# Kernel optimization log

Measured on AMD Instinct MI355X. Metric: run time of the kernel, lower is better.

Reference implementation:

```python
import jax, jax.numpy as jnp
import numpy as np

DIST_THRESH = 0.5   # stands in for config.dist_thresh
ALPHA = 0.2         # LeakyReLU negative slope
NEG_INF = -9e15     # mask value used by the original module


def setup_inputs() -> dict:
    key = jax.random.key(0)
    k1, k2, k3 = jax.random.split(key, 3)
    N, dim = 8192, 128
    nodes = jax.random.normal(k1, (N, dim), dtype=jnp.float32)
    dist = jax.random.uniform(k2, (N, N), dtype=jnp.float32)
    # xavier_uniform on (2*dim, 1) with gain 1.414
    limit = 1.414 * np.sqrt(6.0 / (2 * dim + 1))
    a = jax.random.uniform(k3, (2 * dim, 1), dtype=jnp.float32,
                           minval=-limit, maxval=limit)
    return {"nodes": nodes, "dist": dist, "a": a}


def reference(nodes, dist, a):
    # Original math: e_ij = leakyrelu([h_i || h_j] @ a). Since a = [a1; a2],
    # this equals leakyrelu(h_i @ a1 + h_j @ a2) — same values, no N^2*2dim tensor.
    dim = nodes.shape[1]
    a1 = a[:dim, 0]                      # [dim]
    a2 = a[dim:, 0]                      # [dim]
    s1 = nodes @ a1                      # [N] — contribution of row node i
    s2 = nodes @ a2                      # [N] — contribution of col node j
    e = jax.nn.leaky_relu(s1[:, None] + s2[None, :], negative_slope=ALPHA)  # [N, N]
    masked = jnp.where(dist < DIST_THRESH, e, NEG_INF)
    attention = jax.nn.softmax(masked, axis=1)   # [N, N]
    h_prime = attention @ nodes                  # [N, dim]
    return h_prime
```

## Files before the change

kernel.cpp:

```cpp
#include <hip/hip_runtime.h>
#include <stdint.h>

#define NN 8192
#define DIM 128
#define ALPHA 0.2f
#define MTILE 32
#define BTHREADS 512

typedef float f32x16 __attribute__((ext_vector_type(16)));
typedef short bf16x8 __attribute__((ext_vector_type(8)));

__device__ __forceinline__ float b2f(uint32_t u){
  uint32_t x = u << 16;
  float f;
  __builtin_memcpy(&f, &x, 4);
  return f;
}
__device__ __forceinline__ uint16_t f2b(float f){
  uint32_t x;
  __builtin_memcpy(&x, &f, 4);
  x += 0x7FFFu + ((x >> 16) & 1u);
  return (uint16_t)(x >> 16);
}

__global__ void s_kernel(const float* __restrict__ nodes,
                         const float* __restrict__ a,
                         float* __restrict__ s1, float* __restrict__ s2){
  int row  = blockIdx.x * 4 + (threadIdx.x >> 6);
  int lane = threadIdx.x & 63;
  float2 nv  = *(const float2*)(nodes + row * DIM + lane * 2);
  float2 a1v = *(const float2*)(a + lane * 2);
  float2 a2v = *(const float2*)(a + DIM + lane * 2);
  float p1 = nv.x * a1v.x + nv.y * a1v.y;
  float p2 = nv.x * a2v.x + nv.y * a2v.y;
  #pragma unroll
  for (int off = 32; off; off >>= 1){
    p1 += __shfl_down(p1, off);
    p2 += __shfl_down(p2, off);
  }
  if (lane == 0){ s1[row] = p1; s2[row] = p2; }
}

__global__ void t_kernel(const float* __restrict__ nodes,
                         uint16_t* __restrict__ nodesT){
  __shared__ uint16_t tile[32][33];
  int kb = blockIdx.x * 32, nb = blockIdx.y * 32;
  int tx = threadIdx.x & 31, ty = threadIdx.x >> 5;
  for (int r = ty; r < 32; r += 8)
    tile[r][tx] = f2b(nodes[(size_t)(kb + r) * DIM + nb + tx]);
  __syncthreads();
  for (int r = ty; r < 32; r += 8)
    nodesT[(size_t)(nb + r) * NN + kb + tx] = tile[tx][r];
}

__global__ void __launch_bounds__(BTHREADS)
attn_kernel(const float* __restrict__ dist,
            const uint16_t* __restrict__ nodesT,
            const float* __restrict__ s1,
            const float* __restrict__ s2,
            float* __restrict__ out){
  const int tid  = threadIdx.x;
  const int wave = tid >> 6;
  const int lane = tid & 63;
  const int m    = lane & 31;
  const int half = lane >> 5;
  const int i0   = blockIdx.x * MTILE;

  const float s1v = s1[i0 + m];

  const int kwave = NN / (BTHREADS / 64);
  const int kbeg  = wave * kwave;
  const int steps = kwave / 16;

  f32x16 acc0, acc1, acc2, acc3;
  #pragma unroll
  for (int i = 0; i < 16; i++){ acc0[i] = 0.f; acc1[i] = 0.f; acc2[i] = 0.f; acc3[i] = 0.f; }
  float den = 0.f;

  const float*    dp  = dist   + (size_t)(i0 + m) * NN + kbeg + half * 8;
  const float*    sp  = s2     + kbeg + half * 8;
  const uint16_t* b0p = nodesT + (size_t)m * NN + kbeg + half * 8;
  const uint16_t* b1p = b0p + (size_t)32 * NN;
  const uint16_t* b2p = b0p + (size_t)64 * NN;
  const uint16_t* b3p = b0p + (size_t)96 * NN;

  for (int s = 0; s < steps; s++){
    float4 da  = *(const float4*)dp;
    float4 db  = *(const float4*)(dp + 4);
    float4 sa  = *(const float4*)sp;
    float4 sb  = *(const float4*)(sp + 4);
    uint4  nb0 = *(const uint4*)b0p;
    uint4  nb1 = *(const uint4*)b1p;
    uint4  nb2 = *(const uint4*)b2p;
    uint4  nb3 = *(const uint4*)b3p;

    float dv[8]  = {da.x, da.y, da.z, da.w, db.x, db.y, db.z, db.w};
    float s2v[8] = {sa.x, sa.y, sa.z, sa.w, sb.x, sb.y, sb.z, sb.w};

    union { bf16x8 v; uint16_t u[8]; } af;
    #pragma unroll
    for (int j = 0; j < 8; j++){
      float x = s1v + s2v[j];
      float e = fmaxf(x, ALPHA * x);
      float w = (dv[j] < 0.5f) ? __expf(e) : 0.f;
      uint16_t wq = f2b(w);
      af.u[j] = wq;
      den += b2f((uint32_t)wq);
    }

    acc0 = __builtin_amdgcn_mfma_f32_32x32x16_bf16(af.v, *(const bf16x8*)&nb0, acc0, 0, 0, 0);
    acc1 = __builtin_amdgcn_mfma_f32_32x32x16_bf16(af.v, *(const bf16x8*)&nb1, acc1, 0, 0, 0);
    acc2 = __builtin_amdgcn_mfma_f32_32x32x16_bf16(af.v, *(const bf16x8*)&nb2, acc2, 0, 0, 0);
    acc3 = __builtin_amdgcn_mfma_f32_32x32x16_bf16(af.v, *(const bf16x8*)&nb3, acc3, 0, 0, 0);

    dp  += 16; sp  += 16;
    b0p += 16; b1p += 16; b2p += 16; b3p += 16;
  }

  __shared__ float accT[MTILE][DIM];
  __shared__ float denT[MTILE];
  for (int idx = tid; idx < MTILE * DIM; idx += BTHREADS) ((float*)accT)[idx] = 0.f;
  if (tid < MTILE) denT[tid] = 0.f;
  __syncthreads();

  #pragma unroll
  for (int r = 0; r < 16; r++){
    int row = (r & 3) + 8 * (r >> 2) + 4 * half;
    atomicAdd(&accT[row][ 0 + m], acc0[r]);
    atomicAdd(&accT[row][32 + m], acc1[r]);
    atomicAdd(&accT[row][64 + m], acc2[r]);
    atomicAdd(&accT[row][96 + m], acc3[r]);
  }
  atomicAdd(&denT[m], den);
  __syncthreads();

  if (tid < MTILE) denT[tid] = 1.0f / denT[tid];
  __syncthreads();

  for (int idx = tid; idx < MTILE * DIM; idx += BTHREADS){
    int row = idx >> 7, col = idx & 127;
    out[(size_t)(i0 + row) * DIM + col] = accT[row][col] * denT[row];
  }
}

extern "C" void kernel_launch(void* const* d_in, const int* in_sizes, int n_in,
                              void* d_out, int out_size, void* d_ws, size_t ws_size,
                              hipStream_t stream){
  const float* nodes = (const float*)d_in[0];
  const float* dist  = (const float*)d_in[1];
  const float* a     = (const float*)d_in[2];
  float* out = (float*)d_out;

  char* ws = (char*)d_ws;
  float*    s1     = (float*)ws;
  float*    s2     = (float*)(ws + (32 << 10));
  uint16_t* nodesT = (uint16_t*)(ws + (64 << 10));

  s_kernel<<<NN / 4, 256, 0, stream>>>(nodes, a, s1, s2);
  t_kernel<<<dim3(NN / 32, DIM / 32), 256, 0, stream>>>(nodes, nodesT);
  attn_kernel<<<NN / MTILE, BTHREADS, 0, stream>>>(dist, nodesT, s1, s2, out);
}
```

Measured before the change: 471.6 us.

## Split the K dimension of the attention kernel across blocks with global atomic reduction

Adds a second grid dimension that splits the 8192-long key range into four chunks, so the attention kernel launches four times as many blocks. Each block reduces its partial numerator and denominator into global buffers with atomics, and a new normalization kernel divides afterwards. Two zero-fill kernels clear those buffers first. The aim is better occupancy and latency hiding on the dist stream, at the cost of global atomic traffic, extra launches and a non-deterministic summation order.

```diff
diff --git a/kernel.cpp b/kernel.cpp
--- a/kernel.cpp
+++ b/kernel.cpp
@@ -6,6 +6,7 @@
 #define ALPHA 0.2f
 #define MTILE 32
 #define BTHREADS 512
+#define KSPLIT 4
 
 typedef float f32x16 __attribute__((ext_vector_type(16)));
 typedef short bf16x8 __attribute__((ext_vector_type(8)));
@@ -21,6 +22,11 @@
   __builtin_memcpy(&x, &f, 4);
   x += 0x7FFFu + ((x >> 16) & 1u);
   return (uint16_t)(x >> 16);
+}
+
+__global__ void zero_kernel(float* __restrict__ p, int n){
+  int i = blockIdx.x * 256 + threadIdx.x;
+  if (i < n) p[i] = 0.f;
 }
 
 __global__ void s_kernel(const float* __restrict__ nodes,
@@ -58,18 +64,21 @@
             const uint16_t* __restrict__ nodesT,
             const float* __restrict__ s1,
             const float* __restrict__ s2,
-            float* __restrict__ out){
+            float* __restrict__ acc_g,
+            float* __restrict__ den_g){
   const int tid  = threadIdx.x;
   const int wave = tid >> 6;
   const int lane = tid & 63;
   const int m    = lane & 31;
   const int half = lane >> 5;
   const int i0   = blockIdx.x * MTILE;
+  const int kb   = blockIdx.y;
 
   const float s1v = s1[i0 + m];
 
-  const int kwave = NN / (BTHREADS / 64);
-  const int kbeg  = wave * kwave;
+  const int kblk  = NN / KSPLIT;
+  const int kwave = kblk / (BTHREADS / 64);
+  const int kbeg  = kb * kblk + wave * kwave;
   const int steps = kwave / 16;
 
   f32x16 acc0, acc1, acc2, acc3;
@@ -134,13 +143,18 @@
   atomicAdd(&denT[m], den);
   __syncthreads();
 
-  if (tid < MTILE) denT[tid] = 1.0f / denT[tid];
-  __syncthreads();
+  float* ag = acc_g + (size_t)i0 * DIM;
+  for (int idx = tid; idx < MTILE * DIM; idx += BTHREADS)
+    atomicAdd(&ag[idx], ((float*)accT)[idx]);
+  if (tid < MTILE) atomicAdd(&den_g[i0 + tid], denT[tid]);
+}
 
-  for (int idx = tid; idx < MTILE * DIM; idx += BTHREADS){
-    int row = idx >> 7, col = idx & 127;
-    out[(size_t)(i0 + row) * DIM + col] = accT[row][col] * denT[row];
-  }
+__global__ void norm_kernel(const float* __restrict__ acc_g,
+                            const float* __restrict__ den_g,
+                            float* __restrict__ out){
+  int gid = blockIdx.x * 256 + threadIdx.x;
+  int row = gid >> 7;
+  out[gid] = acc_g[gid] / den_g[row];
 }
 
 extern "C" void kernel_launch(void* const* d_in, const int* in_sizes, int n_in,
@@ -155,8 +169,15 @@
   float*    s1     = (float*)ws;
   float*    s2     = (float*)(ws + (32 << 10));
   uint16_t* nodesT = (uint16_t*)(ws + (64 << 10));
+  float*    acc_g  = (float*)(ws + (64 << 10) + (2 << 20));
+  float*    den_g  = (float*)(ws + (64 << 10) + (6 << 20));
 
+  const int nz = NN * DIM + NN;
+  (void)nz;
+  zero_kernel<<<(NN * DIM + 255) / 256, 256, 0, stream>>>(acc_g, NN * DIM);
+  zero_kernel<<<(NN + 255) / 256, 256, 0, stream>>>(den_g, NN);
   s_kernel<<<NN / 4, 256, 0, stream>>>(nodes, a, s1, s2);
   t_kernel<<<dim3(NN / 32, DIM / 32), 256, 0, stream>>>(nodes, nodesT);
-  attn_kernel<<<NN / MTILE, BTHREADS, 0, stream>>>(dist, nodesT, s1, s2, out);
+  attn_kernel<<<dim3(NN / MTILE, KSPLIT), BTHREADS, 0, stream>>>(dist, nodesT, s1, s2, acc_g, den_g);
+  norm_kernel<<<NN * DIM / 256, 256, 0, stream>>>(acc_g, den_g, out);
 }
```

Measured after the change: 527.7 us. 11.9% more time.

## Stage attention weights in shared memory with double-buffered chunks and per-wave column split

Applied to the files above, without the earlier changes.

Attention weights for each 32-row tile are now computed once per 256-column chunk by all threads and written as bf16 into a double-buffered LDS tile. Each wave then covers one 32-column slice of the output and half of each chunk, reading weights from LDS and nodesT from global memory. Before, every wave recomputed its own weights and ran four MFMAs per step. The change removes the k-split LDS atomic reduction in favour of a two-wave add and a shuffle-based denominator sum. It adds a barrier per chunk, and each thread now does more exp work per chunk.

```diff
diff --git a/kernel.cpp b/kernel.cpp
--- a/kernel.cpp
+++ b/kernel.cpp
@@ -6,6 +6,9 @@
 #define ALPHA 0.2f
 #define MTILE 32
 #define BTHREADS 512
+#define BK 256
+#define NCHUNK (NN / BK)
+#define WSTRIDE (BK + 8)
 
 typedef float f32x16 __attribute__((ext_vector_type(16)));
 typedef short bf16x8 __attribute__((ext_vector_type(8)));
@@ -59,87 +62,113 @@
             const float* __restrict__ s1,
             const float* __restrict__ s2,
             float* __restrict__ out){
+  __shared__ uint16_t Wbuf[2][MTILE][WSTRIDE];
+  __shared__ float accT[MTILE][DIM];
+  __shared__ float denT[MTILE];
+
   const int tid  = threadIdx.x;
+  const int lane = tid & 63;
   const int wave = tid >> 6;
-  const int lane = tid & 63;
+  const int i0   = blockIdx.x * MTILE;
+
+  const int wrow = tid >> 4;
+  const int wr   = tid & 15;
+  const float s1v = s1[i0 + wrow];
+  const float* distRow = dist + (size_t)(i0 + wrow) * NN + wr * 8;
+
+  const int q    = wave & 3;
+  const int h    = wave >> 2;
   const int m    = lane & 31;
   const int half = lane >> 5;
-  const int i0   = blockIdx.x * MTILE;
+  const uint16_t* bRow = nodesT + (size_t)(q * 32 + m) * NN;
 
-  const float s1v = s1[i0 + m];
-
-  const int kwave = NN / (BTHREADS / 64);
-  const int kbeg  = wave * kwave;
-  const int steps = kwave / 16;
-
-  f32x16 acc0, acc1, acc2, acc3;
+  f32x16 acc;
   #pragma unroll
-  for (int i = 0; i < 16; i++){ acc0[i] = 0.f; acc1[i] = 0.f; acc2[i] = 0.f; acc3[i] = 0.f; }
+  for (int i = 0; i < 16; i++) acc[i] = 0.f;
   float den = 0.f;
 
-  const float*    dp  = dist   + (size_t)(i0 + m) * NN + kbeg + half * 8;
-  const float*    sp  = s2     + kbeg + half * 8;
-  const uint16_t* b0p = nodesT + (size_t)m * NN + kbeg + half * 8;
-  const uint16_t* b1p = b0p + (size_t)32 * NN;
-  const uint16_t* b2p = b0p + (size_t)64 * NN;
-  const uint16_t* b3p = b0p + (size_t)96 * NN;
+  float4 pd0, pd1, pd2, pd3, ps0, ps1, ps2, ps3;
 
-  for (int s = 0; s < steps; s++){
-    float4 da  = *(const float4*)dp;
-    float4 db  = *(const float4*)(dp + 4);
-    float4 sa  = *(const float4*)sp;
-    float4 sb  = *(const float4*)(sp + 4);
-    uint4  nb0 = *(const uint4*)b0p;
-    uint4  nb1 = *(const uint4*)b1p;
-    uint4  nb2 = *(const uint4*)b2p;
-    uint4  nb3 = *(const uint4*)b3p;
+  auto load_chunk = [&](int s){
+    const float* dpp = distRow + s * BK;
+    const float* spp = s2 + s * BK + wr * 8;
+    pd0 = *(const float4*)(dpp);
+    pd1 = *(const float4*)(dpp + 4);
+    pd2 = *(const float4*)(dpp + 128);
+    pd3 = *(const float4*)(dpp + 132);
+    ps0 = *(const float4*)(spp);
+    ps1 = *(const float4*)(spp + 4);
+    ps2 = *(const float4*)(spp + 128);
+    ps3 = *(const float4*)(spp + 132);
+  };
 
-    float dv[8]  = {da.x, da.y, da.z, da.w, db.x, db.y, db.z, db.w};
-    float s2v[8] = {sa.x, sa.y, sa.z, sa.w, sb.x, sb.y, sb.z, sb.w};
-
-    union { bf16x8 v; uint16_t u[8]; } af;
+  auto gen_write = [&](int buf){
+    float dv[16] = {pd0.x, pd0.y, pd0.z, pd0.w, pd1.x, pd1.y, pd1.z, pd1.w,
+                    pd2.x, pd2.y, pd2.z, pd2.w, pd3.x, pd3.y, pd3.z, pd3.w};
+    float sv[16] = {ps0.x, ps0.y, ps0.z, ps0.w, ps1.x, ps1.y, ps1.z, ps1.w,
+                    ps2.x, ps2.y, ps2.z, ps2.w, ps3.x, ps3.y, ps3.z, ps3.w};
+    union { bf16x8 v; uint16_t u[8]; } w0, w1;
     #pragma unroll
     for (int j = 0; j < 8; j++){
-      float x = s1v + s2v[j];
+      float x = s1v + sv[j];
       float e = fmaxf(x, ALPHA * x);
       float w = (dv[j] < 0.5f) ? __expf(e) : 0.f;
       uint16_t wq = f2b(w);
-      af.u[j] = wq;
+      w0.u[j] = wq;
       den += b2f((uint32_t)wq);
     }
+    #pragma unroll
+    for (int j = 0; j < 8; j++){
+      float x = s1v + sv[8 + j];
+      float e = fmaxf(x, ALPHA * x);
+      float w = (dv[8 + j] < 0.5f) ? __expf(e) : 0.f;
+      uint16_t wq = f2b(w);
+      w1.u[j] = wq;
+      den += b2f((uint32_t)wq);
+    }
+    *(bf16x8*)&Wbuf[buf][wrow][wr * 8]       = w0.v;
+    *(bf16x8*)&Wbuf[buf][wrow][wr * 8 + 128] = w1.v;
+  };
 
-    acc0 = __builtin_amdgcn_mfma_f32_32x32x16_bf16(af.v, *(const bf16x8*)&nb0, acc0, 0, 0, 0);
-    acc1 = __builtin_amdgcn_mfma_f32_32x32x16_bf16(af.v, *(const bf16x8*)&nb1, acc1, 0, 0, 0);
-    acc2 = __builtin_amdgcn_mfma_f32_32x32x16_bf16(af.v, *(const bf16x8*)&nb2, acc2, 0, 0, 0);
-    acc3 = __builtin_amdgcn_mfma_f32_32x32x16_bf16(af.v, *(const bf16x8*)&nb3, acc3, 0, 0, 0);
+  load_chunk(0);
+  gen_write(0);
 
-    dp  += 16; sp  += 16;
-    b0p += 16; b1p += 16; b2p += 16; b3p += 16;
+  for (int s = 0; s < NCHUNK; s++){
+    if (s + 1 < NCHUNK) load_chunk(s + 1);
+    __syncthreads();
+    const int buf = s & 1;
+    const size_t kb = (size_t)s * BK;
+    #pragma unroll
+    for (int kk = 0; kk < 8; kk++){
+      int ko = h * 128 + kk * 16 + half * 8;
+      bf16x8 av = *(const bf16x8*)&Wbuf[buf][m][ko];
+      bf16x8 bv = *(const bf16x8*)(bRow + kb + ko);
+      acc = __builtin_amdgcn_mfma_f32_32x32x16_bf16(av, bv, acc, 0, 0, 0);
+    }
+    if (s + 1 < NCHUNK) gen_write((s + 1) & 1);
   }
 
-  __shared__ float accT[MTILE][DIM];
-  __shared__ float denT[MTILE];
-  for (int idx = tid; idx < MTILE * DIM; idx += BTHREADS) ((float*)accT)[idx] = 0.f;
-  if (tid < MTILE) denT[tid] = 0.f;
+  den += __shfl_down(den, 8, 16);
+  den += __shfl_down(den, 4, 16);
+  den += __shfl_down(den, 2, 16);
+  den += __shfl_down(den, 1, 16);
+  if (wr == 0) denT[wrow] = 1.0f / den;
+
+  if (h == 0){
+    #pragma unroll
+    for (int r = 0; r < 16; r++){
+      int row = (r & 3) + 8 * (r >> 2) + 4 * half;
+      accT[row][q * 32 + m] = acc[r];
+    }
+  }
   __syncthreads();
-
-  #pragma unroll
-  for (int r = 0; r < 16; r++){
-    int row = (r & 3) + 8 * (r >> 2) + 4 * half;
-    atomicAdd(&accT[row][ 0 + m], acc0[r]);
-    atomicAdd(&accT[row][32 + m], acc1[r]);
-    atomicAdd(&accT[row][64 + m], acc2[r]);
-    atomicAdd(&accT[row][96 + m], acc3[r]);
-  }
-  atomicAdd(&denT[m], den);
-  __syncthreads();
-
-  if (tid < MTILE) denT[tid] = 1.0f / denT[tid];
-  __syncthreads();
-
-  for (int idx = tid; idx < MTILE * DIM; idx += BTHREADS){
-    int row = idx >> 7, col = idx & 127;
-    out[(size_t)(i0 + row) * DIM + col] = accT[row][col] * denT[row];
+  if (h == 1){
+    #pragma unroll
+    for (int r = 0; r < 16; r++){
+      int row = (r & 3) + 8 * (r >> 2) + 4 * half;
+      float v = (accT[row][q * 32 + m] + acc[r]) * denT[row];
+      out[(size_t)(i0 + row) * DIM + q * 32 + m] = v;
+    }
   }
 }
 
```

New measurement: 394.7 us. -16.3%, faster.
